# Optimization experiments

Measured on AMD Instinct MI355X. Metric: run time of the kernel, lower is better.

## Reference

```python
import jax, jax.numpy as jnp
import numpy as np

D, K = 256, 6            # input_dim, n_thresh_per_feat
T, DEPTH = 256, 6        # n_trees, depth
C = 8                    # output_dim
FIN = 2 * D * K          # 3072
B = 4096


def sparsemax(z, axis=-1):
    """Euclidean projection of z onto the probability simplex along `axis`."""
    z = jnp.moveaxis(z, axis, -1)
    zs = jnp.flip(jnp.sort(z, axis=-1), axis=-1)          # descending
    csum = jnp.cumsum(zs, axis=-1)
    r = jnp.arange(1, z.shape[-1] + 1, dtype=z.dtype)
    support = 1.0 + r * zs > csum                          # bool
    k = jnp.sum(support, axis=-1, keepdims=True)           # support size (int)
    tau = (jnp.take_along_axis(csum, k - 1, axis=-1) - 1.0) / k.astype(z.dtype)
    out = jnp.maximum(z - tau, 0.0)
    return jnp.moveaxis(out, -1, axis)


def setup_inputs() -> dict:
    key = jax.random.key(0)
    ks = jax.random.split(key, 5)
    return {
        "x": jax.random.normal(ks[0], (B, D), jnp.float32),
        "thr": jax.random.normal(ks[1], (D, K), jnp.float32),
        "log_beta": jnp.zeros((D, K), jnp.float32),
        "sel_logits": 0.01 * jax.random.normal(ks[2], (T * DEPTH, FIN), jnp.float32),
        "leaf_value": 0.01 * jax.random.normal(ks[3], (T, 2 ** DEPTH, C), jnp.float32),
        "att_W": 0.01 * jax.random.normal(ks[4], (FIN, T), jnp.float32),
        "att_b": jnp.zeros((T,), jnp.float32),
    }


def reference(x, thr, log_beta, sel_logits, leaf_value, att_W, att_b):
    b = x.shape[0]
    t = leaf_value.shape[0]
    depth = sel_logits.shape[0] // t
    # ThresholdFactBank: smooth per-(feature,threshold) facts in (0,1)
    f = jax.nn.sigmoid((x[:, :, None] - thr[None]) * jnp.exp(log_beta)[None])
    f = f.reshape(b, -1)                                   # (B, F0)
    f_aug = jnp.concatenate([f, 1.0 - f], axis=1)          # (B, Fin)
    # sparsemax feature selection per (tree, level)
    sel = sparsemax(sel_logits, axis=1).reshape(t, depth, -1)
    p = jnp.clip(jnp.einsum('bf,tdf->btd', f_aug, sel), 1e-6, 1.0 - 1e-6)
    # recursive leaf-probability doubling
    probs = jnp.ones((b, t, 1), x.dtype)
    for d in range(depth):
        pd = p[:, :, d:d + 1]                              # (B, T, 1)
        probs = jnp.concatenate([probs * (1.0 - pd), probs * pd], axis=2)
    # per-tree outputs and sparsemax attention pooling over trees
    y_t = jnp.einsum('btl,tlc->btc', probs, leaf_value)    # (B, T, C)
    a = sparsemax(f_aug @ att_W + att_b, axis=1)           # (B, T)
    return jnp.sum(a[:, :, None] * y_t, axis=1)            # (B, C)
```

## Files before the change

### kernel.cpp

```cpp
#include <hip/hip_runtime.h>
#include <cstdint>

#define B_     4096
#define D_     256
#define KK_    6
#define T_     256
#define DEPTH_ 6
#define C_     8
#define F1     1536
#define F2     3072
#define NROW   1536
#define NALL   1792
#define BK     64
#define NIT    (F1 / BK)
#define NFB    24
#define NBLK   448
#define PRE_PREP  96
#define PRE_SEL   (PRE_PREP + 384)
#define PRE_F     (PRE_SEL + 1024)

using bf16x8 = __attribute__((ext_vector_type(8))) __bf16;
using f32x4  = __attribute__((ext_vector_type(4))) float;

__device__ inline float waveSum(float v) {
#pragma unroll
  for (int m = 32; m; m >>= 1) v += __shfl_xor(v, m, 64);
  return v;
}
__device__ inline int waveSumI(int v) {
#pragma unroll
  for (int m = 32; m; m >>= 1) v += __shfl_xor(v, m, 64);
  return v;
}

__device__ __forceinline__ void gload_lds16(const void* g, void* l) {
  __builtin_amdgcn_global_load_lds(
      (const __attribute__((address_space(1))) unsigned int*)g,
      (__attribute__((address_space(3))) unsigned int*)l, 16, 0, 0);
}

__global__ __launch_bounds__(256) void fused_pre_kernel(
    const float* __restrict__ att_W, const float* __restrict__ sel_logits,
    const float* __restrict__ x, const float* __restrict__ thr,
    const float* __restrict__ log_beta,
    __bf16* __restrict__ w_all, float* __restrict__ w_c,
    float* __restrict__ pc, __bf16* __restrict__ f_hi)
{
  const int bid = blockIdx.x;
  if (bid < PRE_PREP) {
    __shared__ float Wl[64][65], Wh[64][65];
    const int fblk = (bid % NFB) * 64;
    const int tblk = (bid / NFB) * 64;
    const int tt = threadIdx.x & 63;
    const int f4 = threadIdx.x >> 6;
#pragma unroll
    for (int r = 0; r < 16; ++r) {
      const int f = r * 4 + f4;
      Wl[f][tt] = att_W[(size_t)(fblk + f) * T_ + tblk + tt];
      Wh[f][tt] = att_W[(size_t)(fblk + f + F1) * T_ + tblk + tt];
    }
    __syncthreads();
    const int t  = threadIdx.x >> 2;
    const int fq = threadIdx.x & 3;
#pragma unroll
    for (int pass = 0; pass < 4; ++pass) {
      const int f0 = pass * 16 + fq * 4;
      alignas(8) __bf16 hv[4];
#pragma unroll
      for (int e = 0; e < 4; ++e)
        hv[e] = (__bf16)(Wl[f0 + e][t] - Wh[f0 + e][t]);
      *(uint2*)&w_all[(size_t)(tblk + t) * F1 + fblk + f0] = *(const uint2*)hv;
    }
    if (threadIdx.x < 64) {
      float s = 0.f;
#pragma unroll
      for (int f = 0; f < 64; ++f) s += Wh[f][threadIdx.x];
      pc[(size_t)(bid % NFB) * T_ + tblk + threadIdx.x] = s;
    }
  } else if (bid < PRE_SEL) {
    const int row  = (bid - PRE_PREP) * 4 + (threadIdx.x >> 6);
    const int lane = threadIdx.x & 63;
    const float* src = sel_logits + (size_t)row * F2;
    float4 z[12];
#pragma unroll
    for (int q = 0; q < 12; ++q)
      z[q] = *(const float4*)(src + q * 256 + lane * 4);

    float tau = -1e30f, taun = 0.f;
    int cprev = F2 + 1;
    for (int it = 0; it < 64; ++it) {
      float s = 0.f; int c = 0;
#pragma unroll
      for (int q = 0; q < 12; ++q) {
        const float* zq = (const float*)&z[q];
#pragma unroll
        for (int r = 0; r < 4; ++r) {
          const float v = zq[r];
          if (v > tau) { s += v; c++; }
        }
      }
      s = waveSum(s); c = waveSumI(c);
      taun = (s - 1.0f) / (float)c;
      if (c == cprev) break;
      cprev = c; tau = taun;
    }
    tau = taun;

    float chi = 0.f;
    __bf16* wrow = w_all + (size_t)(T_ + row) * F1;
#pragma unroll
    for (int q = 0; q < 6; ++q) {
      const float* zlo = (const float*)&z[q];
      const float* zhi = (const float*)&z[q + 6];
      alignas(8) __bf16 wv[4];
#pragma unroll
      for (int r = 0; r < 4; ++r) {
        float lo = zlo[r] - tau; lo = lo > 0.f ? lo : 0.f;
        float hi = zhi[r] - tau; hi = hi > 0.f ? hi : 0.f;
        chi += hi;
        wv[r] = (__bf16)(lo - hi);
      }
      *(uint2*)&wrow[q * 256 + lane * 4] = *(const uint2*)wv;
    }
    const float csum = waveSum(chi);
    if (lane == 0) w_c[row] = csum;
  } else {
    const int base_b = (bid - PRE_SEL) * 4;
    const int d = threadIdx.x;
    float beta[KK_], th[KK_];
#pragma unroll
    for (int k = 0; k < KK_; ++k) {
      beta[k] = __expf(log_beta[d * KK_ + k]);
      th[k]   = thr[d * KK_ + k];
    }
#pragma unroll
    for (int j = 0; j < 4; ++j) {
      const int b = base_b + j;
      const float xv = x[(size_t)b * D_ + d];
      alignas(4) __bf16 hv[6];
#pragma unroll
      for (int k = 0; k < KK_; ++k) {
        const float tt = (xv - th[k]) * beta[k];
        const float s = 1.0f / (1.0f + __expf(-tt));
        hv[k] = (__bf16)s;
      }
      const size_t base = (size_t)b * F1 + d * KK_;
      const unsigned* hp = (const unsigned*)hv;
      unsigned* dh = (unsigned*)&f_hi[base];
      dh[0] = hp[0]; dh[1] = hp[1]; dh[2] = hp[2];
    }
  }
}

__global__ __launch_bounds__(256) void catt_kernel(
    const float* __restrict__ pc, const float* __restrict__ att_b,
    float* __restrict__ catt)
{
  const int t = threadIdx.x;
  float s = att_b[t];
  for (int i = 0; i < NFB; ++i) s += pc[(size_t)i * T_ + t];
  catt[t] = s;
}

__global__ __launch_bounds__(512) void gemm_mfma_kernel(
    const __bf16* __restrict__ f_hi, const __bf16* __restrict__ w_all,
    float* __restrict__ P)
{
  __shared__ __bf16 As[2][128 * 64];
  __shared__ __bf16 Bs[2][128 * 64];
  const int linear = blockIdx.x;
  const int xcd  = linear & 7;
  const int slot = linear >> 3;
  const int bm = (((xcd & 3) << 3) + (slot & 7)) * 128;
  const int bn = (((xcd >> 2) * 7) + (slot >> 3)) * 128;
  const int tid = threadIdx.x;
  const int wid = tid >> 6, lane = tid & 63;
  const int wr = wid >> 2, wc = wid & 3;

  const int srow = lane >> 3;
  const int skb8 = ((lane & 7) ^ srow) << 3;

  const int l15   = lane & 15;
  const int mask  = (lane & 7) << 4;
  const int khalf = (lane >> 4) << 4;
  int offA[4][2], offB[2][2];
#pragma unroll
  for (int m = 0; m < 4; ++m) {
    const int row = wr * 64 + m * 16 + l15;
#pragma unroll
    for (int s = 0; s < 2; ++s)
      offA[m][s] = row * 128 + (((s << 6) | khalf) ^ mask);
  }
#pragma unroll
  for (int n = 0; n < 2; ++n) {
    const int col = wc * 32 + n * 16 + l15;
#pragma unroll
    for (int s = 0; s < 2; ++s)
      offB[n][s] = col * 128 + (((s << 6) | khalf) ^ mask);
  }

  f32x4 acc[4][2] = {};

  auto stage = [&](int it, int buf) {
    const int kl = it * BK;
#pragma unroll
    for (int j = 0; j < 2; ++j) {
      const int q = wid * 2 + j;
      gload_lds16(f_hi  + (size_t)(bm + q * 8 + srow) * F1 + kl + skb8, &As[buf][q * 512]);
      gload_lds16(w_all + (size_t)(bn + q * 8 + srow) * F1 + kl + skb8, &Bs[buf][q * 512]);
    }
  };

  stage(0, 0);
  stage(1, 1);
  for (int it = 0; it < NIT; ++it) {
    const int cur = it & 1;
    if (it + 1 < NIT) asm volatile("s_waitcnt vmcnt(4)" ::: "memory");
    else              asm volatile("s_waitcnt vmcnt(0)" ::: "memory");
    __builtin_amdgcn_sched_barrier(0);
    __builtin_amdgcn_s_barrier();
    __builtin_amdgcn_sched_barrier(0);

    const char* pa = (const char*)As[cur];
    const char* pb = (const char*)Bs[cur];
    __builtin_amdgcn_s_setprio(1);
#pragma unroll
    for (int s = 0; s < 2; ++s) {
      bf16x8 av[4], bv[2];
#pragma unroll
      for (int m = 0; m < 4; ++m) av[m] = *(const bf16x8*)(pa + offA[m][s]);
#pragma unroll
      for (int n = 0; n < 2; ++n) bv[n] = *(const bf16x8*)(pb + offB[n][s]);
#pragma unroll
      for (int m = 0; m < 4; ++m)
#pragma unroll
        for (int n = 0; n < 2; ++n)
          acc[m][n] = __builtin_amdgcn_mfma_f32_16x16x32_bf16(av[m], bv[n], acc[m][n], 0, 0, 0);
    }
    __builtin_amdgcn_s_setprio(0);
    __builtin_amdgcn_sched_barrier(0);
    __builtin_amdgcn_s_barrier();
    __builtin_amdgcn_sched_barrier(0);
    if (it + 2 < NIT) stage(it + 2, cur);
  }

  const int r0 = (lane >> 4) << 2;
#pragma unroll
  for (int m = 0; m < 4; ++m)
#pragma unroll
    for (int n = 0; n < 2; ++n)
#pragma unroll
      for (int r = 0; r < 4; ++r)
        P[(size_t)(bm + wr * 64 + m * 16 + r0 + r) * NALL + (bn + wc * 32 + n * 16 + l15)] =
            acc[m][n][r];
}

__global__ __launch_bounds__(256) void epilogue_kernel(
    const float* __restrict__ P, const float* __restrict__ catt,
    const float* __restrict__ w_c,
    const float* __restrict__ leaf, float* __restrict__ out)
{
  const int b = blockIdx.x;
  __shared__ float a_val_sh[T_];
  __shared__ unsigned short a_t_sh[T_];
  __shared__ int nact_sh;
  __shared__ float oacc[4][C_];
  const int tid = threadIdx.x;
  const int wid = tid >> 6, lane = tid & 63;

  if (wid == 0) {
    float z[4];
#pragma unroll
    for (int j = 0; j < 4; ++j) {
      const int t = lane + 64 * j;
      z[j] = P[(size_t)b * NALL + t] + catt[t];
    }
    float tau = -1e30f, taun = 0.f;
    int cprev = T_ + 1;
    for (int it = 0; it < 40; ++it) {
      float s = 0.f; int c = 0;
#pragma unroll
      for (int j = 0; j < 4; ++j) if (z[j] > tau) { s += z[j]; c++; }
      s = waveSum(s); c = waveSumI(c);
      taun = (s - 1.0f) / (float)c;
      if (c == cprev) break;
      cprev = c; tau = taun;
    }
    tau = taun;
    float av[4]; int nnz = 0;
#pragma unroll
    for (int j = 0; j < 4; ++j) {
      float a = z[j] - tau; av[j] = a > 0.f ? a : 0.f;
      if (av[j] > 0.f) nnz++;
    }
    int incl = nnz;
#pragma unroll
    for (int off = 1; off < 64; off <<= 1) {
      const int n = __shfl_up(incl, off, 64);
      if (lane >= off) incl += n;
    }
    int pos = incl - nnz;
#pragma unroll
    for (int j = 0; j < 4; ++j) {
      if (av[j] > 0.f) {
        a_val_sh[pos] = av[j];
        a_t_sh[pos] = (unsigned short)(lane + 64 * j);
        pos++;
      }
    }
    if (lane == 63) nact_sh = incl;
  }
  __syncthreads();

  const int nact = nact_sh;
  float o[C_];
#pragma unroll
  for (int c = 0; c < C_; ++c) o[c] = 0.f;

  for (int i = wid; i < nact; i += 4) {
    const int t = (int)a_t_sh[i];
    const float* pp = P + (size_t)b * NALL + T_ + t * DEPTH_;
    const float* wc = w_c + t * DEPTH_;
    float prob = a_val_sh[i];
#pragma unroll
    for (int d = 0; d < DEPTH_; ++d) {
      float pv = wc[d] + pp[d];
      pv = pv < 1e-6f ? 1e-6f : (pv > 1.0f - 1e-6f ? 1.0f - 1e-6f : pv);
      prob *= ((lane >> d) & 1) ? pv : (1.0f - pv);
    }
    const float* lf = leaf + ((size_t)t * 64 + lane) * C_;
#pragma unroll
    for (int c = 0; c < C_; ++c) o[c] += prob * lf[c];
  }
#pragma unroll
  for (int c = 0; c < C_; ++c) o[c] = waveSum(o[c]);
  if (lane == 0) {
#pragma unroll
    for (int c = 0; c < C_; ++c) oacc[wid][c] = o[c];
  }
  __syncthreads();
  if (tid < C_)
    out[(size_t)b * C_ + tid] = oacc[0][tid] + oacc[1][tid] + oacc[2][tid] + oacc[3][tid];
}

extern "C" void kernel_launch(void* const* d_in, const int* in_sizes, int n_in,
                              void* d_out, int out_size, void* d_ws, size_t ws_size,
                              hipStream_t stream)
{
  const float* x        = (const float*)d_in[0];
  const float* thr      = (const float*)d_in[1];
  const float* log_beta = (const float*)d_in[2];
  const float* sel      = (const float*)d_in[3];
  const float* leaf     = (const float*)d_in[4];
  const float* att_W    = (const float*)d_in[5];
  const float* att_b    = (const float*)d_in[6];
  float* out = (float*)d_out;

  char* ws = (char*)d_ws;
  size_t off = 0;
  auto alloc = [&](size_t bytes) {
    char* p = ws + off;
    off = (off + bytes + 255) & ~(size_t)255;
    return p;
  };
  __bf16* f_hi   = (__bf16*)alloc((size_t)B_ * F1 * 2);
  __bf16* w_all  = (__bf16*)alloc((size_t)NALL * F1 * 2);
  float*  catt   = (float*)alloc((size_t)T_ * 4);
  float*  pc     = (float*)alloc((size_t)NFB * T_ * 4);
  float*  w_c    = (float*)alloc((size_t)NROW * 4);
  float*  P      = (float*)alloc((size_t)B_ * NALL * 4);
  (void)ws_size; (void)in_sizes; (void)n_in; (void)out_size;

  hipLaunchKernelGGL(fused_pre_kernel, dim3(PRE_F),  dim3(256), 0, stream,
                     att_W, sel, x, thr, log_beta, w_all, w_c, pc, f_hi);
  hipLaunchKernelGGL(catt_kernel,      dim3(1),      dim3(256), 0, stream, pc, att_b, catt);
  hipLaunchKernelGGL(gemm_mfma_kernel, dim3(NBLK),   dim3(512), 0, stream, f_hi, w_all, P);
  hipLaunchKernelGGL(epilogue_kernel,  dim3(B_),     dim3(256), 0, stream, P, catt, w_c, leaf, out);
}
```

Before: 66.49 us.

## Fold catt into epilogue, one wave per row, warm-start sparsemax iterations

Removes the single-block catt kernel and recomputes the attention bias sum (24 partials plus att_b) inside the epilogue. The epilogue now handles one batch row per wave instead of one per block, using ballot and shuffle to walk active trees instead of a shared-memory compaction and two block syncs. Both sparsemax threshold loops start from the full-set mean tau, which skips one reduction iteration. The trade-off is that every wave redundantly reads 24×256 pc values, and each row's active-tree work now runs serially on a single wave.

```diff
diff --git a/kernel.cpp b/kernel.cpp
--- a/kernel.cpp
+++ b/kernel.cpp
@@ -82,13 +82,16 @@
     const int lane = threadIdx.x & 63;
     const float* src = sel_logits + (size_t)row * F2;
     float4 z[12];
-#pragma unroll
-    for (int q = 0; q < 12; ++q)
+    float s_all = 0.f;
+#pragma unroll
+    for (int q = 0; q < 12; ++q) {
       z[q] = *(const float4*)(src + q * 256 + lane * 4);
-
-    float tau = -1e30f, taun = 0.f;
-    int cprev = F2 + 1;
-    for (int it = 0; it < 64; ++it) {
+      s_all += z[q].x + z[q].y + z[q].z + z[q].w;
+    }
+    float tau = (waveSum(s_all) - 1.0f) / (float)F2;
+    float taun = tau;
+    int cprev = F2;
+    for (int it = 0; it < 63; ++it) {
       float s = 0.f; int c = 0;
 #pragma unroll
       for (int q = 0; q < 12; ++q) {
@@ -150,16 +153,6 @@
       dh[0] = hp[0]; dh[1] = hp[1]; dh[2] = hp[2];
     }
   }
-}
-
-__global__ __launch_bounds__(256) void catt_kernel(
-    const float* __restrict__ pc, const float* __restrict__ att_b,
-    float* __restrict__ catt)
-{
-  const int t = threadIdx.x;
-  float s = att_b[t];
-  for (int i = 0; i < NFB; ++i) s += pc[(size_t)i * T_ + t];
-  catt[t] = s;
 }
 
 __global__ __launch_bounds__(512) void gemm_mfma_kernel(
@@ -256,91 +249,75 @@
 }
 
 __global__ __launch_bounds__(256) void epilogue_kernel(
-    const float* __restrict__ P, const float* __restrict__ catt,
-    const float* __restrict__ w_c,
+    const float* __restrict__ P, const float* __restrict__ pc,
+    const float* __restrict__ att_b, const float* __restrict__ w_c,
     const float* __restrict__ leaf, float* __restrict__ out)
 {
-  const int b = blockIdx.x;
-  __shared__ float a_val_sh[T_];
-  __shared__ unsigned short a_t_sh[T_];
-  __shared__ int nact_sh;
-  __shared__ float oacc[4][C_];
-  const int tid = threadIdx.x;
-  const int wid = tid >> 6, lane = tid & 63;
-
-  if (wid == 0) {
-    float z[4];
-#pragma unroll
-    for (int j = 0; j < 4; ++j) {
-      const int t = lane + 64 * j;
-      z[j] = P[(size_t)b * NALL + t] + catt[t];
-    }
-    float tau = -1e30f, taun = 0.f;
-    int cprev = T_ + 1;
-    for (int it = 0; it < 40; ++it) {
-      float s = 0.f; int c = 0;
-#pragma unroll
-      for (int j = 0; j < 4; ++j) if (z[j] > tau) { s += z[j]; c++; }
-      s = waveSum(s); c = waveSumI(c);
-      taun = (s - 1.0f) / (float)c;
-      if (c == cprev) break;
-      cprev = c; tau = taun;
-    }
-    tau = taun;
-    float av[4]; int nnz = 0;
-#pragma unroll
-    for (int j = 0; j < 4; ++j) {
-      float a = z[j] - tau; av[j] = a > 0.f ? a : 0.f;
-      if (av[j] > 0.f) nnz++;
-    }
-    int incl = nnz;
-#pragma unroll
-    for (int off = 1; off < 64; off <<= 1) {
-      const int n = __shfl_up(incl, off, 64);
-      if (lane >= off) incl += n;
-    }
-    int pos = incl - nnz;
-#pragma unroll
-    for (int j = 0; j < 4; ++j) {
-      if (av[j] > 0.f) {
-        a_val_sh[pos] = av[j];
-        a_t_sh[pos] = (unsigned short)(lane + 64 * j);
-        pos++;
+  const int b = blockIdx.x * 4 + (threadIdx.x >> 6);
+  const int lane = threadIdx.x & 63;
+
+  float z[4];
+  float s_all = 0.f;
+#pragma unroll
+  for (int j = 0; j < 4; ++j) {
+    const int t = lane + 64 * j;
+    float cv = att_b[t];
+#pragma unroll
+    for (int i = 0; i < NFB; ++i) cv += pc[(size_t)i * T_ + t];
+    z[j] = P[(size_t)b * NALL + t] + cv;
+    s_all += z[j];
+  }
+  float tau = (waveSum(s_all) - 1.0f) / (float)T_;
+  float taun = tau;
+  int cprev = T_;
+  for (int it = 0; it < 39; ++it) {
+    float s = 0.f; int c = 0;
+#pragma unroll
+    for (int j = 0; j < 4; ++j) if (z[j] > tau) { s += z[j]; c++; }
+    s = waveSum(s); c = waveSumI(c);
+    taun = (s - 1.0f) / (float)c;
+    if (c == cprev) break;
+    cprev = c; tau = taun;
+  }
+  tau = taun;
+  float av[4];
+#pragma unroll
+  for (int j = 0; j < 4; ++j) {
+    const float a = z[j] - tau;
+    av[j] = a > 0.f ? a : 0.f;
+  }
+
+  float o[C_];
+#pragma unroll
+  for (int c = 0; c < C_; ++c) o[c] = 0.f;
+#pragma unroll
+  for (int j = 0; j < 4; ++j) {
+    unsigned long long msk = __ballot(av[j] > 0.f);
+    while (msk) {
+      const int src = (int)__ffsll((long long)msk) - 1;
+      msk &= msk - 1;
+      const float a = __shfl(av[j], src, 64);
+      const int t = src + 64 * j;
+      const float* pp = P + (size_t)b * NALL + T_ + t * DEPTH_;
+      const float* wc = w_c + t * DEPTH_;
+      float prob = a;
+#pragma unroll
+      for (int d = 0; d < DEPTH_; ++d) {
+        float pv = wc[d] + pp[d];
+        pv = pv < 1e-6f ? 1e-6f : (pv > 1.0f - 1e-6f ? 1.0f - 1e-6f : pv);
+        prob *= ((lane >> d) & 1) ? pv : (1.0f - pv);
       }
-    }
-    if (lane == 63) nact_sh = incl;
-  }
-  __syncthreads();
-
-  const int nact = nact_sh;
-  float o[C_];
-#pragma unroll
-  for (int c = 0; c < C_; ++c) o[c] = 0.f;
-
-  for (int i = wid; i < nact; i += 4) {
-    const int t = (int)a_t_sh[i];
-    const float* pp = P + (size_t)b * NALL + T_ + t * DEPTH_;
-    const float* wc = w_c + t * DEPTH_;
-    float prob = a_val_sh[i];
-#pragma unroll
-    for (int d = 0; d < DEPTH_; ++d) {
-      float pv = wc[d] + pp[d];
-      pv = pv < 1e-6f ? 1e-6f : (pv > 1.0f - 1e-6f ? 1.0f - 1e-6f : pv);
-      prob *= ((lane >> d) & 1) ? pv : (1.0f - pv);
-    }
-    const float* lf = leaf + ((size_t)t * 64 + lane) * C_;
-#pragma unroll
-    for (int c = 0; c < C_; ++c) o[c] += prob * lf[c];
+      const float* lf = leaf + ((size_t)t * 64 + lane) * C_;
+#pragma unroll
+      for (int c = 0; c < C_; ++c) o[c] += prob * lf[c];
+    }
   }
 #pragma unroll
   for (int c = 0; c < C_; ++c) o[c] = waveSum(o[c]);
   if (lane == 0) {
 #pragma unroll
-    for (int c = 0; c < C_; ++c) oacc[wid][c] = o[c];
-  }
-  __syncthreads();
-  if (tid < C_)
-    out[(size_t)b * C_ + tid] = oacc[0][tid] + oacc[1][tid] + oacc[2][tid] + oacc[3][tid];
+    for (int c = 0; c < C_; ++c) out[(size_t)b * C_ + c] = o[c];
+  }
 }
 
 extern "C" void kernel_launch(void* const* d_in, const int* in_sizes, int n_in,
@@ -365,7 +342,6 @@
   };
   __bf16* f_hi   = (__bf16*)alloc((size_t)B_ * F1 * 2);
   __bf16* w_all  = (__bf16*)alloc((size_t)NALL * F1 * 2);
-  float*  catt   = (float*)alloc((size_t)T_ * 4);
   float*  pc     = (float*)alloc((size_t)NFB * T_ * 4);
   float*  w_c    = (float*)alloc((size_t)NROW * 4);
   float*  P      = (float*)alloc((size_t)B_ * NALL * 4);
@@ -373,7 +349,7 @@
 
   hipLaunchKernelGGL(fused_pre_kernel, dim3(PRE_F),  dim3(256), 0, stream,
                      att_W, sel, x, thr, log_beta, w_all, w_c, pc, f_hi);
-  hipLaunchKernelGGL(catt_kernel,      dim3(1),      dim3(256), 0, stream, pc, att_b, catt);
   hipLaunchKernelGGL(gemm_mfma_kernel, dim3(NBLK),   dim3(512), 0, stream, f_hi, w_all, P);
-  hipLaunchKernelGGL(epilogue_kernel,  dim3(B_),     dim3(256), 0, stream, P, catt, w_c, leaf, out);
-}
+  hipLaunchKernelGGL(epilogue_kernel,  dim3(B_ / 4), dim3(256), 0, stream,
+                     P, pc, att_b, w_c, leaf, out);
+}
```

Measured after the change: 59.19 us. -11.0%, faster.
